# Performance work log

Measured on AMD Instinct MI355X. Metric: run time of the kernel, lower is better.

The kernel has to match this reference:

```python
import jax, jax.numpy as jnp
import numpy as np

T, H, I, E, S = 1024, 1024, 512, 64, 2  # tokens, hidden, intermediate, routed experts, shared experts
G, TOPK_GROUP, K = 8, 4, 8              # n_group, topk_group, num_experts_per_tok


def setup_inputs() -> dict:
    key = jax.random.key(0)
    ks = jax.random.split(key, 6)
    scale = 0.02
    x = jax.random.normal(ks[0], (T, H), dtype=jnp.float32)
    gate_w = jax.random.normal(ks[1], (E, H), dtype=jnp.float32) * scale   # MoEGate.weight [E,H]
    w_gu = jax.random.normal(ks[2], (E, H, 2 * I), dtype=jnp.float32) * scale  # gate_up_proj.weight.T per expert
    w_d = jax.random.normal(ks[3], (E, I, H), dtype=jnp.float32) * scale       # down_proj.weight.T per expert
    s_gu = jax.random.normal(ks[4], (S, H, 2 * I), dtype=jnp.float32) * scale  # shared experts
    s_d = jax.random.normal(ks[5], (S, I, H), dtype=jnp.float32) * scale
    return {"x": x, "gate_w": gate_w, "w_gu": w_gu, "w_d": w_d, "s_gu": s_gu, "s_d": s_d}


def _moe_forward(x, gate_w, w_gu, w_d, s_gu, s_d):
    t, h = x.shape
    e = w_gu.shape[0]
    i = w_gu.shape[2] // 2
    group_size = e // G

    # ---- shared experts (always active), summed ----
    sh = jnp.einsum('th,shf->stf', x, s_gu)            # [S,T,2I]
    shared = jnp.einsum('stf,sfh->th', jax.nn.silu(sh[..., :i]) * sh[..., i:], s_d)

    # ---- grouped top-k gating ----
    logits = x @ gate_w.T                               # [T,E]
    group_logits = logits.reshape(t, G, group_size)
    gw, gi = jax.lax.top_k(group_logits, TOPK_GROUP)    # [T,G,topk_group]
    gw = gw.reshape(t, G * TOPK_GROUP)
    gi = gi.reshape(t, G * TOPK_GROUP)
    topk_w, ti = jax.lax.top_k(gw, K)                   # [T,K]
    sel_group = ti // TOPK_GROUP
    expert_in_group = jnp.take_along_axis(gi, ti, axis=1)
    topk_idx = sel_group * group_size + expert_in_group # [T,K]
    topk_w = topk_w / (topk_w.sum(axis=-1, keepdims=True) + 1e-20)  # norm_topk_prob

    # ---- combine weights: sparse [T,E] scatter of top-k weights ----
    combine = jnp.zeros((t, e), x.dtype).at[jnp.arange(t)[:, None], topk_idx].add(topk_w)

    # ---- routed experts: dense grouped GEMM, zero-weighted where unselected ----
    gu = jnp.einsum('th,ehf->etf', x, w_gu)             # [E,T,2I]
    hidden = jax.nn.silu(gu[..., :i]) * gu[..., i:]     # [E,T,I]
    y = jnp.einsum('eti,eih->eth', hidden, w_d)         # [E,T,H]
    routed = jnp.einsum('eth,te->th', y, combine)

    return shared + routed


def reference(x, gate_w, w_gu, w_d, s_gu, s_d):
    return _moe_forward(x, gate_w, w_gu, w_d, s_gu, s_d)
```

## Files before the change

kernel.cpp:

```cpp
#include <hip/hip_runtime.h>
#include <hip/hip_bf16.h>

#define T_ 1024
#define H_ 1024
#define I_ 512
#define E_ 64
#define S_ 2
#define NJOB 66
#define KSEL 8
#define GRP 8
#define GSIZE 8
#define TKG 4
#define ROWS_TOTAL (T_*KSEL + S_*T_)

#define BM 128
#define BN 64
#define BK 32
#define LDA 40
#define LDB 40

typedef __attribute__((ext_vector_type(8))) __bf16 bf16x8;
typedef __attribute__((ext_vector_type(4))) float f32x4;

__device__ inline unsigned short f2bf(float f) {
    unsigned u = __float_as_uint(f);
    u += 0x7FFFu + ((u >> 16) & 1u);
    return (unsigned short)(u >> 16);
}

__global__ __launch_bounds__(256) void cvt_x_kernel(const float* __restrict__ x,
                                                    unsigned short* __restrict__ xb) {
    int i = (blockIdx.x * 256 + threadIdx.x) * 4;
    float4 v = *(const float4*)(x + i);
    ushort4 o;
    o.x = f2bf(v.x); o.y = f2bf(v.y); o.z = f2bf(v.z); o.w = f2bf(v.w);
    *(ushort4*)(xb + i) = o;
}

__global__ __launch_bounds__(64) void gate_kernel(const float* __restrict__ x,
                                                  const float* __restrict__ gate_w,
                                                  int* __restrict__ counts,
                                                  int* __restrict__ topk_idx,
                                                  float* __restrict__ topk_w) {
    int t = blockIdx.x;
    int e = threadIdx.x;
    const float4* xr = (const float4*)(x + (size_t)t * H_);
    const float4* wr = (const float4*)(gate_w + (size_t)e * H_);
    float acc = 0.0f;
    for (int i = 0; i < H_ / 4; ++i) {
        float4 a = xr[i], b = wr[i];
        acc += a.x * b.x + a.y * b.y + a.z * b.z + a.w * b.w;
    }
    __shared__ float lg[E_];
    lg[e] = acc;
    __syncthreads();
    if (e == 0) {
        float cv[GRP * TKG];
        int   ce[GRP * TKG];
        for (int g = 0; g < GRP; ++g) {
            unsigned used = 0;
            for (int r = 0; r < TKG; ++r) {
                float best = -INFINITY; int bi = 0;
                for (int j = 0; j < GSIZE; ++j) {
                    if (used & (1u << j)) continue;
                    float v = lg[g * GSIZE + j];
                    if (v > best) { best = v; bi = j; }
                }
                used |= 1u << bi;
                cv[g * TKG + r] = best;
                ce[g * TKG + r] = g * GSIZE + bi;
            }
        }
        float sv[KSEL]; int si[KSEL];
        unsigned used = 0;
        float sum = 0.0f;
        for (int r = 0; r < KSEL; ++r) {
            float best = -INFINITY; int bi = 0;
            for (int j = 0; j < GRP * TKG; ++j) {
                if (used & (1u << j)) continue;
                if (cv[j] > best) { best = cv[j]; bi = j; }
            }
            used |= 1u << bi;
            sv[r] = best; si[r] = ce[bi];
            sum += best;
        }
        float inv = 1.0f / (sum + 1e-20f);
        for (int r = 0; r < KSEL; ++r) {
            topk_idx[t * KSEL + r] = si[r];
            topk_w[t * KSEL + r] = sv[r] * inv;
            atomicAdd(&counts[si[r]], 1);
        }
    }
}

__global__ void prefix_kernel(int* __restrict__ counts, int* __restrict__ offsets,
                              int* __restrict__ cursor) {
    if (threadIdx.x == 0) {
        counts[E_] = T_;
        counts[E_ + 1] = T_;
        int acc = 0;
        for (int j = 0; j < NJOB; ++j) {
            offsets[j] = acc;
            cursor[j] = acc;
            acc += counts[j];
        }
        offsets[NJOB] = acc;
    }
}

__global__ __launch_bounds__(256) void place_kernel(const int* __restrict__ topk_idx,
                                                    const float* __restrict__ topk_w,
                                                    const int* __restrict__ offsets,
                                                    int* __restrict__ cursor,
                                                    int* __restrict__ row_token,
                                                    float* __restrict__ row_w) {
    int p = blockIdx.x * 256 + threadIdx.x;
    if (p < T_ * KSEL) {
        int t = p >> 3;
        int e = topk_idx[p];
        int slot = atomicAdd(&cursor[e], 1);
        row_token[slot] = t;
        row_w[slot] = topk_w[p];
    } else if (p < T_ * KSEL + S_ * T_) {
        int q = p - T_ * KSEL;
        int s = q >> 10;
        int t = q & (T_ - 1);
        int slot = offsets[E_ + s] + t;
        row_token[slot] = t;
        row_w[slot] = 1.0f;
    }
}

__global__ __launch_bounds__(256) void gateup_kernel(const unsigned short* __restrict__ xb,
                                                     const float* __restrict__ w_gu,
                                                     const float* __restrict__ s_gu,
                                                     const int* __restrict__ offsets,
                                                     const int* __restrict__ row_token,
                                                     unsigned short* __restrict__ hidden) {
    int job = blockIdx.x, mt = blockIdx.y, nt = blockIdx.z;
    int seg = offsets[job];
    int cnt = offsets[job + 1] - seg;
    int m0 = mt * BM;
    if (m0 >= cnt) return;
    const float* Bp = (job < E_) ? (w_gu + (size_t)job * H_ * (2 * I_))
                                 : (s_gu + (size_t)(job - E_) * H_ * (2 * I_));
    int n0 = nt * BN;

    __shared__ unsigned short As[BM * LDA];
    __shared__ unsigned short Bg[BN * LDB];
    __shared__ unsigned short Bu[BN * LDB];

    int tid = threadIdx.x;
    int wv = tid >> 6;
    int lane = tid & 63;
    int lrow = lane & 15;
    int lq = lane >> 4;

    int arow0 = tid >> 2;
    int akc = (tid & 3) * 8;
    int arow1 = (tid + 256) >> 2;
    int gidx0 = seg + m0 + arow0; if (gidx0 > ROWS_TOTAL - 1) gidx0 = ROWS_TOTAL - 1;
    int gidx1 = seg + m0 + arow1; if (gidx1 > ROWS_TOTAL - 1) gidx1 = ROWS_TOTAL - 1;
    const unsigned short* ap0 = xb + (size_t)row_token[gidx0] * H_;
    const unsigned short* ap1 = xb + (size_t)row_token[gidx1] * H_;

    int bk0 = tid >> 4;
    int bnc = (tid & 15) * 4;
    int bk1 = bk0 + 16;

    f32x4 accg[2][4], accu[2][4];
    f32x4 zero = {0.f, 0.f, 0.f, 0.f};
#pragma unroll
    for (int a = 0; a < 2; ++a)
#pragma unroll
        for (int b = 0; b < 4; ++b) { accg[a][b] = zero; accu[a][b] = zero; }

    for (int k0 = 0; k0 < H_; k0 += BK) {
        *(uint4*)&As[arow0 * LDA + akc] = *(const uint4*)(ap0 + k0 + akc);
        *(uint4*)&As[arow1 * LDA + akc] = *(const uint4*)(ap1 + k0 + akc);

        float4 vg0 = *(const float4*)(Bp + (size_t)(k0 + bk0) * (2 * I_) + n0 + bnc);
        float4 vg1 = *(const float4*)(Bp + (size_t)(k0 + bk1) * (2 * I_) + n0 + bnc);
        float4 vu0 = *(const float4*)(Bp + (size_t)(k0 + bk0) * (2 * I_) + (I_ + n0) + bnc);
        float4 vu1 = *(const float4*)(Bp + (size_t)(k0 + bk1) * (2 * I_) + (I_ + n0) + bnc);
        Bg[(bnc + 0) * LDB + bk0] = f2bf(vg0.x);
        Bg[(bnc + 1) * LDB + bk0] = f2bf(vg0.y);
        Bg[(bnc + 2) * LDB + bk0] = f2bf(vg0.z);
        Bg[(bnc + 3) * LDB + bk0] = f2bf(vg0.w);
        Bg[(bnc + 0) * LDB + bk1] = f2bf(vg1.x);
        Bg[(bnc + 1) * LDB + bk1] = f2bf(vg1.y);
        Bg[(bnc + 2) * LDB + bk1] = f2bf(vg1.z);
        Bg[(bnc + 3) * LDB + bk1] = f2bf(vg1.w);
        Bu[(bnc + 0) * LDB + bk0] = f2bf(vu0.x);
        Bu[(bnc + 1) * LDB + bk0] = f2bf(vu0.y);
        Bu[(bnc + 2) * LDB + bk0] = f2bf(vu0.z);
        Bu[(bnc + 3) * LDB + bk0] = f2bf(vu0.w);
        Bu[(bnc + 0) * LDB + bk1] = f2bf(vu1.x);
        Bu[(bnc + 1) * LDB + bk1] = f2bf(vu1.y);
        Bu[(bnc + 2) * LDB + bk1] = f2bf(vu1.z);
        Bu[(bnc + 3) * LDB + bk1] = f2bf(vu1.w);
        __syncthreads();

#pragma unroll
        for (int rb = 0; rb < 2; ++rb) {
            bf16x8 af = *(const bf16x8*)&As[(wv * 32 + rb * 16 + lrow) * LDA + lq * 8];
#pragma unroll
            for (int cb = 0; cb < 4; ++cb) {
                bf16x8 bg = *(const bf16x8*)&Bg[(cb * 16 + lrow) * LDB + lq * 8];
                bf16x8 bu = *(const bf16x8*)&Bu[(cb * 16 + lrow) * LDB + lq * 8];
                accg[rb][cb] = __builtin_amdgcn_mfma_f32_16x16x32_bf16(af, bg, accg[rb][cb], 0, 0, 0);
                accu[rb][cb] = __builtin_amdgcn_mfma_f32_16x16x32_bf16(af, bu, accu[rb][cb], 0, 0, 0);
            }
        }
        __syncthreads();
    }

#pragma unroll
    for (int rb = 0; rb < 2; ++rb) {
#pragma unroll
        for (int cb = 0; cb < 4; ++cb) {
#pragma unroll
            for (int r = 0; r < 4; ++r) {
                int row = wv * 32 + rb * 16 + lq * 4 + r;
                if (m0 + row < cnt) {
                    float g = accg[rb][cb][r];
                    float u = accu[rb][cb][r];
                    float h = g / (1.0f + __expf(-g)) * u;
                    int col = n0 + cb * 16 + lrow;
                    hidden[(size_t)(seg + m0 + row) * I_ + col] = f2bf(h);
                }
            }
        }
    }
}

__global__ __launch_bounds__(256) void down_kernel(const unsigned short* __restrict__ hidden,
                                                   const float* __restrict__ w_d,
                                                   const float* __restrict__ s_d,
                                                   const int* __restrict__ offsets,
                                                   const int* __restrict__ row_token,
                                                   const float* __restrict__ row_w,
                                                   float* __restrict__ out) {
    int job = blockIdx.x, mt = blockIdx.y, nt = blockIdx.z;
    int seg = offsets[job];
    int cnt = offsets[job + 1] - seg;
    int m0 = mt * BM;
    if (m0 >= cnt) return;
    const float* Bp = (job < E_) ? (w_d + (size_t)job * I_ * H_)
                                 : (s_d + (size_t)(job - E_) * I_ * H_);
    int n0 = nt * BN;

    __shared__ unsigned short As[BM * LDA];
    __shared__ unsigned short Bs[BN * LDB];

    int tid = threadIdx.x;
    int wv = tid >> 6;
    int lane = tid & 63;
    int lrow = lane & 15;
    int lq = lane >> 4;

    int arow0 = tid >> 2;
    int akc = (tid & 3) * 8;
    int arow1 = (tid + 256) >> 2;
    int gidx0 = seg + m0 + arow0; if (gidx0 > ROWS_TOTAL - 1) gidx0 = ROWS_TOTAL - 1;
    int gidx1 = seg + m0 + arow1; if (gidx1 > ROWS_TOTAL - 1) gidx1 = ROWS_TOTAL - 1;
    const unsigned short* ap0 = hidden + (size_t)gidx0 * I_;
    const unsigned short* ap1 = hidden + (size_t)gidx1 * I_;

    int bk0 = tid >> 4;
    int bnc = (tid & 15) * 4;
    int bk1 = bk0 + 16;

    f32x4 acc[2][4];
    f32x4 zero = {0.f, 0.f, 0.f, 0.f};
#pragma unroll
    for (int a = 0; a < 2; ++a)
#pragma unroll
        for (int b = 0; b < 4; ++b) acc[a][b] = zero;

    for (int k0 = 0; k0 < I_; k0 += BK) {
        *(uint4*)&As[arow0 * LDA + akc] = *(const uint4*)(ap0 + k0 + akc);
        *(uint4*)&As[arow1 * LDA + akc] = *(const uint4*)(ap1 + k0 + akc);

        float4 v0 = *(const float4*)(Bp + (size_t)(k0 + bk0) * H_ + n0 + bnc);
        float4 v1 = *(const float4*)(Bp + (size_t)(k0 + bk1) * H_ + n0 + bnc);
        Bs[(bnc + 0) * LDB + bk0] = f2bf(v0.x);
        Bs[(bnc + 1) * LDB + bk0] = f2bf(v0.y);
        Bs[(bnc + 2) * LDB + bk0] = f2bf(v0.z);
        Bs[(bnc + 3) * LDB + bk0] = f2bf(v0.w);
        Bs[(bnc + 0) * LDB + bk1] = f2bf(v1.x);
        Bs[(bnc + 1) * LDB + bk1] = f2bf(v1.y);
        Bs[(bnc + 2) * LDB + bk1] = f2bf(v1.z);
        Bs[(bnc + 3) * LDB + bk1] = f2bf(v1.w);
        __syncthreads();

#pragma unroll
        for (int rb = 0; rb < 2; ++rb) {
            bf16x8 af = *(const bf16x8*)&As[(wv * 32 + rb * 16 + lrow) * LDA + lq * 8];
#pragma unroll
            for (int cb = 0; cb < 4; ++cb) {
                bf16x8 bf = *(const bf16x8*)&Bs[(cb * 16 + lrow) * LDB + lq * 8];
                acc[rb][cb] = __builtin_amdgcn_mfma_f32_16x16x32_bf16(af, bf, acc[rb][cb], 0, 0, 0);
            }
        }
        __syncthreads();
    }

#pragma unroll
    for (int rb = 0; rb < 2; ++rb) {
#pragma unroll
        for (int cb = 0; cb < 4; ++cb) {
#pragma unroll
            for (int r = 0; r < 4; ++r) {
                int row = wv * 32 + rb * 16 + lq * 4 + r;
                if (m0 + row < cnt) {
                    int gi = seg + m0 + row;
                    float v = acc[rb][cb][r] * row_w[gi];
                    atomicAdd(&out[(size_t)row_token[gi] * H_ + n0 + cb * 16 + lrow], v);
                }
            }
        }
    }
}

extern "C" void kernel_launch(void* const* d_in, const int* in_sizes, int n_in,
                              void* d_out, int out_size, void* d_ws, size_t ws_size,
                              hipStream_t stream) {
    const float* x      = (const float*)d_in[0];
    const float* gate_w = (const float*)d_in[1];
    const float* w_gu   = (const float*)d_in[2];
    const float* w_d    = (const float*)d_in[3];
    const float* s_gu   = (const float*)d_in[4];
    const float* s_d    = (const float*)d_in[5];
    float* out = (float*)d_out;

    char* ws = (char*)d_ws;
    size_t off = 0;
    auto carve = [&](size_t bytes) -> void* {
        void* p = ws + off;
        off += (bytes + 255) & ~(size_t)255;
        return p;
    };
    int* counts            = (int*)carve(NJOB * 4);
    int* offsets           = (int*)carve((NJOB + 1) * 4);
    int* cursor            = (int*)carve(NJOB * 4);
    int* topk_idx          = (int*)carve(T_ * KSEL * 4);
    float* topk_w          = (float*)carve(T_ * KSEL * 4);
    int* row_token         = (int*)carve(ROWS_TOTAL * 4);
    float* row_w           = (float*)carve(ROWS_TOTAL * 4);
    unsigned short* xb     = (unsigned short*)carve((size_t)T_ * H_ * 2);
    unsigned short* hidden = (unsigned short*)carve((size_t)ROWS_TOTAL * I_ * 2);

    hipMemsetAsync(out, 0, (size_t)T_ * H_ * 4, stream);
    hipMemsetAsync(counts, 0, NJOB * 4, stream);

    cvt_x_kernel<<<(T_ * H_ / 4) / 256, 256, 0, stream>>>(x, xb);
    gate_kernel<<<T_, 64, 0, stream>>>(x, gate_w, counts, topk_idx, topk_w);
    prefix_kernel<<<1, 64, 0, stream>>>(counts, offsets, cursor);
    place_kernel<<<(ROWS_TOTAL + 255) / 256, 256, 0, stream>>>(topk_idx, topk_w, offsets,
                                                               cursor, row_token, row_w);
    gateup_kernel<<<dim3(NJOB, T_ / BM, I_ / BN), 256, 0, stream>>>(xb, w_gu, s_gu, offsets,
                                                                    row_token, hidden);
    down_kernel<<<dim3(NJOB, T_ / BM, H_ / BN), 256, 0, stream>>>(hidden, w_d, s_d, offsets,
                                                                  row_token, row_w, out);
}
```

Before: 703.0 us.

## Restructure GEMM kernels with register-prefetched weights, direct A loads, tiled gate

The gate-up and down GEMMs now read activation rows straight from global memory into MFMA registers, with no LDS staging. Weight tiles use BK=64, are prefetched one step ahead into registers, and are stored to LDS as packed vectors with staggered writes. The down kernel loads the token index and weight once per row before the atomic adds. The gate kernel handles four tokens per block and stages a transposed weight tile in LDS. This aims to cut LDS traffic, scalar stores and global latency stalls, at the cost of more registers and uncoalesced direct A loads.

```diff
diff --git a/kernel.cpp b/kernel.cpp
--- a/kernel.cpp
+++ b/kernel.cpp
@@ -15,11 +15,11 @@
 
 #define BM 128
 #define BN 64
-#define BK 32
-#define LDA 40
-#define LDB 40
+#define LDB 72
 
 typedef __attribute__((ext_vector_type(8))) __bf16 bf16x8;
+typedef __attribute__((ext_vector_type(8))) unsigned short u16x8;
+typedef __attribute__((ext_vector_type(4))) unsigned short u16x4;
 typedef __attribute__((ext_vector_type(4))) float f32x4;
 
 __device__ inline unsigned short f2bf(float f) {
@@ -31,30 +31,57 @@
 __global__ __launch_bounds__(256) void cvt_x_kernel(const float* __restrict__ x,
                                                     unsigned short* __restrict__ xb) {
     int i = (blockIdx.x * 256 + threadIdx.x) * 4;
-    float4 v = *(const float4*)(x + i);
-    ushort4 o;
-    o.x = f2bf(v.x); o.y = f2bf(v.y); o.z = f2bf(v.z); o.w = f2bf(v.w);
-    *(ushort4*)(xb + i) = o;
-}
-
-__global__ __launch_bounds__(64) void gate_kernel(const float* __restrict__ x,
-                                                  const float* __restrict__ gate_w,
-                                                  int* __restrict__ counts,
-                                                  int* __restrict__ topk_idx,
-                                                  float* __restrict__ topk_w) {
-    int t = blockIdx.x;
-    int e = threadIdx.x;
-    const float4* xr = (const float4*)(x + (size_t)t * H_);
-    const float4* wr = (const float4*)(gate_w + (size_t)e * H_);
-    float acc = 0.0f;
-    for (int i = 0; i < H_ / 4; ++i) {
-        float4 a = xr[i], b = wr[i];
-        acc += a.x * b.x + a.y * b.y + a.z * b.z + a.w * b.w;
-    }
-    __shared__ float lg[E_];
-    lg[e] = acc;
+    f32x4 v = *(const f32x4*)(x + i);
+    u16x4 o;
+    o[0] = f2bf(v[0]); o[1] = f2bf(v[1]); o[2] = f2bf(v[2]); o[3] = f2bf(v[3]);
+    *(u16x4*)(xb + i) = o;
+}
+
+__global__ __launch_bounds__(256) void gate_kernel(const float* __restrict__ x,
+                                                   const float* __restrict__ gate_w,
+                                                   int* __restrict__ counts,
+                                                   int* __restrict__ topk_idx,
+                                                   float* __restrict__ topk_w) {
+    __shared__ float Wt[64 * 65];
+    __shared__ float Xs[4 * 65];
+    __shared__ float lg[4 * 65];
+
+    int tid = threadIdx.x;
+    int t0 = blockIdx.x * 4;
+    int e = tid & 63;
+    int wq = tid >> 6;
+    int er = tid >> 2;
+    int kq = (tid & 3) * 16;
+    int xk = tid & 63;
+
+    float acc = 0.f;
+    for (int kc = 0; kc < 16; ++kc) {
+        const float* wp = gate_w + er * H_ + kc * 64 + kq;
+        f32x4 w0 = *(const f32x4*)(wp);
+        f32x4 w1 = *(const f32x4*)(wp + 4);
+        f32x4 w2 = *(const f32x4*)(wp + 8);
+        f32x4 w3 = *(const f32x4*)(wp + 12);
+        float xv = x[(size_t)(t0 + wq) * H_ + kc * 64 + xk];
+        __syncthreads();
+#pragma unroll
+        for (int i = 0; i < 4; ++i) {
+            Wt[(kq + i) * 65 + er] = w0[i];
+            Wt[(kq + 4 + i) * 65 + er] = w1[i];
+            Wt[(kq + 8 + i) * 65 + er] = w2[i];
+            Wt[(kq + 12 + i) * 65 + er] = w3[i];
+        }
+        Xs[wq * 65 + xk] = xv;
+        __syncthreads();
+#pragma unroll 8
+        for (int k = 0; k < 64; ++k)
+            acc += Wt[k * 65 + e] * Xs[wq * 65 + k];
+    }
+    lg[wq * 65 + e] = acc;
     __syncthreads();
-    if (e == 0) {
+
+    if (tid < 4) {
+        int t = t0 + tid;
+        const float* L = &lg[tid * 65];
         float cv[GRP * TKG];
         int   ce[GRP * TKG];
         for (int g = 0; g < GRP; ++g) {
@@ -63,7 +90,7 @@
                 float best = -INFINITY; int bi = 0;
                 for (int j = 0; j < GSIZE; ++j) {
                     if (used & (1u << j)) continue;
-                    float v = lg[g * GSIZE + j];
+                    float v = L[g * GSIZE + j];
                     if (v > best) { best = v; bi = j; }
                 }
                 used |= 1u << bi;
@@ -145,93 +172,101 @@
     const float* Bp = (job < E_) ? (w_gu + (size_t)job * H_ * (2 * I_))
                                  : (s_gu + (size_t)(job - E_) * H_ * (2 * I_));
     int n0 = nt * BN;
-
-    __shared__ unsigned short As[BM * LDA];
-    __shared__ unsigned short Bg[BN * LDB];
-    __shared__ unsigned short Bu[BN * LDB];
+    const int N2 = 2 * I_;
+
+    __shared__ unsigned short Bs[2 * BN * LDB];
 
     int tid = threadIdx.x;
-    int wv = tid >> 6;
-    int lane = tid & 63;
-    int lrow = lane & 15;
-    int lq = lane >> 4;
-
-    int arow0 = tid >> 2;
-    int akc = (tid & 3) * 8;
-    int arow1 = (tid + 256) >> 2;
-    int gidx0 = seg + m0 + arow0; if (gidx0 > ROWS_TOTAL - 1) gidx0 = ROWS_TOTAL - 1;
-    int gidx1 = seg + m0 + arow1; if (gidx1 > ROWS_TOTAL - 1) gidx1 = ROWS_TOTAL - 1;
-    const unsigned short* ap0 = xb + (size_t)row_token[gidx0] * H_;
-    const unsigned short* ap1 = xb + (size_t)row_token[gidx1] * H_;
-
-    int bk0 = tid >> 4;
-    int bnc = (tid & 15) * 4;
-    int bk1 = bk0 + 16;
-
-    f32x4 accg[2][4], accu[2][4];
+    int wv = tid >> 6, lane = tid & 63, lrow = lane & 15, lq = lane >> 4;
+
+    const unsigned short* arow[2];
+#pragma unroll
+    for (int rb = 0; rb < 2; ++rb) {
+        int r = m0 + wv * 32 + rb * 16 + lrow;
+        int gi = seg + (r < cnt ? r : 0);
+        arow[rb] = xb + (size_t)row_token[gi] * H_ + lq * 8;
+    }
+
+    int half = tid >> 7;
+    int h = tid & 127;
+    int nb = (h & 15) * 4;
+    int kb = (h >> 4) * 8;
+    const float* bgp = Bp + (size_t)kb * N2 + (half ? (I_ + n0) : n0) + nb;
+    unsigned short* wrow = &Bs[(half * BN + nb) * LDB + kb];
+    int stagger = tid & 3;
+
+    f32x4 acc[2][2][4];
     f32x4 zero = {0.f, 0.f, 0.f, 0.f};
 #pragma unroll
     for (int a = 0; a < 2; ++a)
 #pragma unroll
-        for (int b = 0; b < 4; ++b) { accg[a][b] = zero; accu[a][b] = zero; }
-
-    for (int k0 = 0; k0 < H_; k0 += BK) {
-        *(uint4*)&As[arow0 * LDA + akc] = *(const uint4*)(ap0 + k0 + akc);
-        *(uint4*)&As[arow1 * LDA + akc] = *(const uint4*)(ap1 + k0 + akc);
-
-        float4 vg0 = *(const float4*)(Bp + (size_t)(k0 + bk0) * (2 * I_) + n0 + bnc);
-        float4 vg1 = *(const float4*)(Bp + (size_t)(k0 + bk1) * (2 * I_) + n0 + bnc);
-        float4 vu0 = *(const float4*)(Bp + (size_t)(k0 + bk0) * (2 * I_) + (I_ + n0) + bnc);
-        float4 vu1 = *(const float4*)(Bp + (size_t)(k0 + bk1) * (2 * I_) + (I_ + n0) + bnc);
-        Bg[(bnc + 0) * LDB + bk0] = f2bf(vg0.x);
-        Bg[(bnc + 1) * LDB + bk0] = f2bf(vg0.y);
-        Bg[(bnc + 2) * LDB + bk0] = f2bf(vg0.z);
-        Bg[(bnc + 3) * LDB + bk0] = f2bf(vg0.w);
-        Bg[(bnc + 0) * LDB + bk1] = f2bf(vg1.x);
-        Bg[(bnc + 1) * LDB + bk1] = f2bf(vg1.y);
-        Bg[(bnc + 2) * LDB + bk1] = f2bf(vg1.z);
-        Bg[(bnc + 3) * LDB + bk1] = f2bf(vg1.w);
-        Bu[(bnc + 0) * LDB + bk0] = f2bf(vu0.x);
-        Bu[(bnc + 1) * LDB + bk0] = f2bf(vu0.y);
-        Bu[(bnc + 2) * LDB + bk0] = f2bf(vu0.z);
-        Bu[(bnc + 3) * LDB + bk0] = f2bf(vu0.w);
-        Bu[(bnc + 0) * LDB + bk1] = f2bf(vu1.x);
-        Bu[(bnc + 1) * LDB + bk1] = f2bf(vu1.y);
-        Bu[(bnc + 2) * LDB + bk1] = f2bf(vu1.z);
-        Bu[(bnc + 3) * LDB + bk1] = f2bf(vu1.w);
-        __syncthreads();
-
-#pragma unroll
-        for (int rb = 0; rb < 2; ++rb) {
-            bf16x8 af = *(const bf16x8*)&As[(wv * 32 + rb * 16 + lrow) * LDA + lq * 8];
-#pragma unroll
-            for (int cb = 0; cb < 4; ++cb) {
-                bf16x8 bg = *(const bf16x8*)&Bg[(cb * 16 + lrow) * LDB + lq * 8];
-                bf16x8 bu = *(const bf16x8*)&Bu[(cb * 16 + lrow) * LDB + lq * 8];
-                accg[rb][cb] = __builtin_amdgcn_mfma_f32_16x16x32_bf16(af, bg, accg[rb][cb], 0, 0, 0);
-                accu[rb][cb] = __builtin_amdgcn_mfma_f32_16x16x32_bf16(af, bu, accu[rb][cb], 0, 0, 0);
+        for (int b = 0; b < 2; ++b)
+#pragma unroll
+            for (int c = 0; c < 4; ++c) acc[a][b][c] = zero;
+
+    f32x4 bv[8];
+#pragma unroll
+    for (int j = 0; j < 8; ++j) bv[j] = *(const f32x4*)(bgp + (size_t)j * N2);
+
+    for (int kt = 0; kt < H_ / 64; ++kt) {
+        u16x8 pk[4];
+#pragma unroll
+        for (int c = 0; c < 4; ++c)
+#pragma unroll
+            for (int j = 0; j < 8; ++j) pk[c][j] = f2bf(bv[j][c]);
+        __syncthreads();
+#pragma unroll
+        for (int c0 = 0; c0 < 4; ++c0) {
+            int c = (c0 + stagger) & 3;
+            *(u16x8*)(wrow + c * LDB) = pk[c];
+        }
+        __syncthreads();
+
+        bf16x8 av[2][2];
+#pragma unroll
+        for (int rb = 0; rb < 2; ++rb)
+#pragma unroll
+            for (int kk = 0; kk < 2; ++kk)
+                av[rb][kk] = *(const bf16x8*)(arow[rb] + kt * 64 + kk * 32);
+
+        if (kt + 1 < H_ / 64) {
+#pragma unroll
+            for (int j = 0; j < 8; ++j)
+                bv[j] = *(const f32x4*)(bgp + (size_t)((kt + 1) * 64 + j) * N2);
+        }
+
+#pragma unroll
+        for (int kk = 0; kk < 2; ++kk) {
+#pragma unroll
+            for (int mat = 0; mat < 2; ++mat) {
+                bf16x8 bfr[4];
+#pragma unroll
+                for (int cb = 0; cb < 4; ++cb)
+                    bfr[cb] = *(const bf16x8*)&Bs[(mat * BN + cb * 16 + lrow) * LDB + kk * 32 + lq * 8];
+#pragma unroll
+                for (int rb = 0; rb < 2; ++rb)
+#pragma unroll
+                    for (int cb = 0; cb < 4; ++cb)
+                        acc[rb][mat][cb] = __builtin_amdgcn_mfma_f32_16x16x32_bf16(
+                            av[rb][kk], bfr[cb], acc[rb][mat][cb], 0, 0, 0);
             }
         }
-        __syncthreads();
-    }
-
-#pragma unroll
-    for (int rb = 0; rb < 2; ++rb) {
-#pragma unroll
-        for (int cb = 0; cb < 4; ++cb) {
+    }
+
+#pragma unroll
+    for (int rb = 0; rb < 2; ++rb)
+#pragma unroll
+        for (int cb = 0; cb < 4; ++cb)
 #pragma unroll
             for (int r = 0; r < 4; ++r) {
                 int row = wv * 32 + rb * 16 + lq * 4 + r;
                 if (m0 + row < cnt) {
-                    float g = accg[rb][cb][r];
-                    float u = accu[rb][cb][r];
-                    float h = g / (1.0f + __expf(-g)) * u;
-                    int col = n0 + cb * 16 + lrow;
-                    hidden[(size_t)(seg + m0 + row) * I_ + col] = f2bf(h);
+                    float g = acc[rb][0][cb][r];
+                    float u = acc[rb][1][cb][r];
+                    float hh = g / (1.0f + __expf(-g)) * u;
+                    hidden[(size_t)(seg + m0 + row) * I_ + n0 + cb * 16 + lrow] = f2bf(hh);
                 }
             }
-        }
-    }
 }
 
 __global__ __launch_bounds__(256) void down_kernel(const unsigned short* __restrict__ hidden,
@@ -250,77 +285,96 @@
                                  : (s_d + (size_t)(job - E_) * I_ * H_);
     int n0 = nt * BN;
 
-    __shared__ unsigned short As[BM * LDA];
     __shared__ unsigned short Bs[BN * LDB];
 
     int tid = threadIdx.x;
-    int wv = tid >> 6;
-    int lane = tid & 63;
-    int lrow = lane & 15;
-    int lq = lane >> 4;
-
-    int arow0 = tid >> 2;
-    int akc = (tid & 3) * 8;
-    int arow1 = (tid + 256) >> 2;
-    int gidx0 = seg + m0 + arow0; if (gidx0 > ROWS_TOTAL - 1) gidx0 = ROWS_TOTAL - 1;
-    int gidx1 = seg + m0 + arow1; if (gidx1 > ROWS_TOTAL - 1) gidx1 = ROWS_TOTAL - 1;
-    const unsigned short* ap0 = hidden + (size_t)gidx0 * I_;
-    const unsigned short* ap1 = hidden + (size_t)gidx1 * I_;
-
-    int bk0 = tid >> 4;
-    int bnc = (tid & 15) * 4;
-    int bk1 = bk0 + 16;
+    int wv = tid >> 6, lane = tid & 63, lrow = lane & 15, lq = lane >> 4;
+
+    const unsigned short* arow[2];
+    int arix[2];
+#pragma unroll
+    for (int rb = 0; rb < 2; ++rb) {
+        int r = m0 + wv * 32 + rb * 16 + lrow;
+        int gi = seg + (r < cnt ? r : 0);
+        arow[rb] = hidden + (size_t)gi * I_ + lq * 8;
+        arix[rb] = gi;
+        (void)arix;
+    }
+
+    int nb = (tid & 15) * 4;
+    int kb = (tid >> 4) * 4;
+    const float* bdp = Bp + (size_t)kb * H_ + n0 + nb;
+    unsigned short* wrow = &Bs[nb * LDB + kb];
+    int stagger = tid & 3;
 
     f32x4 acc[2][4];
     f32x4 zero = {0.f, 0.f, 0.f, 0.f};
 #pragma unroll
     for (int a = 0; a < 2; ++a)
 #pragma unroll
-        for (int b = 0; b < 4; ++b) acc[a][b] = zero;
-
-    for (int k0 = 0; k0 < I_; k0 += BK) {
-        *(uint4*)&As[arow0 * LDA + akc] = *(const uint4*)(ap0 + k0 + akc);
-        *(uint4*)&As[arow1 * LDA + akc] = *(const uint4*)(ap1 + k0 + akc);
-
-        float4 v0 = *(const float4*)(Bp + (size_t)(k0 + bk0) * H_ + n0 + bnc);
-        float4 v1 = *(const float4*)(Bp + (size_t)(k0 + bk1) * H_ + n0 + bnc);
-        Bs[(bnc + 0) * LDB + bk0] = f2bf(v0.x);
-        Bs[(bnc + 1) * LDB + bk0] = f2bf(v0.y);
-        Bs[(bnc + 2) * LDB + bk0] = f2bf(v0.z);
-        Bs[(bnc + 3) * LDB + bk0] = f2bf(v0.w);
-        Bs[(bnc + 0) * LDB + bk1] = f2bf(v1.x);
-        Bs[(bnc + 1) * LDB + bk1] = f2bf(v1.y);
-        Bs[(bnc + 2) * LDB + bk1] = f2bf(v1.z);
-        Bs[(bnc + 3) * LDB + bk1] = f2bf(v1.w);
-        __syncthreads();
-
-#pragma unroll
-        for (int rb = 0; rb < 2; ++rb) {
-            bf16x8 af = *(const bf16x8*)&As[(wv * 32 + rb * 16 + lrow) * LDA + lq * 8];
-#pragma unroll
-            for (int cb = 0; cb < 4; ++cb) {
-                bf16x8 bf = *(const bf16x8*)&Bs[(cb * 16 + lrow) * LDB + lq * 8];
-                acc[rb][cb] = __builtin_amdgcn_mfma_f32_16x16x32_bf16(af, bf, acc[rb][cb], 0, 0, 0);
+        for (int c = 0; c < 4; ++c) acc[a][c] = zero;
+
+    f32x4 bv[4];
+#pragma unroll
+    for (int j = 0; j < 4; ++j) bv[j] = *(const f32x4*)(bdp + (size_t)j * H_);
+
+    for (int kt = 0; kt < I_ / 64; ++kt) {
+        u16x4 pk[4];
+#pragma unroll
+        for (int c = 0; c < 4; ++c)
+#pragma unroll
+            for (int j = 0; j < 4; ++j) pk[c][j] = f2bf(bv[j][c]);
+        __syncthreads();
+#pragma unroll
+        for (int c0 = 0; c0 < 4; ++c0) {
+            int c = (c0 + stagger) & 3;
+            *(u16x4*)(wrow + c * LDB) = pk[c];
+        }
+        __syncthreads();
+
+        bf16x8 av[2][2];
+#pragma unroll
+        for (int rb = 0; rb < 2; ++rb)
+#pragma unroll
+            for (int kk = 0; kk < 2; ++kk)
+                av[rb][kk] = *(const bf16x8*)(arow[rb] + kt * 64 + kk * 32);
+
+        if (kt + 1 < I_ / 64) {
+#pragma unroll
+            for (int j = 0; j < 4; ++j)
+                bv[j] = *(const f32x4*)(bdp + (size_t)((kt + 1) * 64 + j) * H_);
+        }
+
+#pragma unroll
+        for (int kk = 0; kk < 2; ++kk) {
+            bf16x8 bfr[4];
+#pragma unroll
+            for (int cb = 0; cb < 4; ++cb)
+                bfr[cb] = *(const bf16x8*)&Bs[(cb * 16 + lrow) * LDB + kk * 32 + lq * 8];
+#pragma unroll
+            for (int rb = 0; rb < 2; ++rb)
+#pragma unroll
+                for (int cb = 0; cb < 4; ++cb)
+                    acc[rb][cb] = __builtin_amdgcn_mfma_f32_16x16x32_bf16(
+                        av[rb][kk], bfr[cb], acc[rb][cb], 0, 0, 0);
+        }
+    }
+
+#pragma unroll
+    for (int rb = 0; rb < 2; ++rb)
+#pragma unroll
+        for (int r = 0; r < 4; ++r) {
+            int row = wv * 32 + rb * 16 + lq * 4 + r;
+            if (m0 + row < cnt) {
+                int gi = seg + m0 + row;
+                int tok = row_token[gi];
+                float w = row_w[gi];
+#pragma unroll
+                for (int cb = 0; cb < 4; ++cb)
+                    atomicAdd(&out[(size_t)tok * H_ + n0 + cb * 16 + lrow],
+                              acc[rb][cb][r] * w);
             }
         }
-        __syncthreads();
-    }
-
-#pragma unroll
-    for (int rb = 0; rb < 2; ++rb) {
-#pragma unroll
-        for (int cb = 0; cb < 4; ++cb) {
-#pragma unroll
-            for (int r = 0; r < 4; ++r) {
-                int row = wv * 32 + rb * 16 + lq * 4 + r;
-                if (m0 + row < cnt) {
-                    int gi = seg + m0 + row;
-                    float v = acc[rb][cb][r] * row_w[gi];
-                    atomicAdd(&out[(size_t)row_token[gi] * H_ + n0 + cb * 16 + lrow], v);
-                }
-            }
-        }
-    }
 }
 
 extern "C" void kernel_launch(void* const* d_in, const int* in_sizes, int n_in,
@@ -355,7 +409,7 @@
     hipMemsetAsync(counts, 0, NJOB * 4, stream);
 
     cvt_x_kernel<<<(T_ * H_ / 4) / 256, 256, 0, stream>>>(x, xb);
-    gate_kernel<<<T_, 64, 0, stream>>>(x, gate_w, counts, topk_idx, topk_w);
+    gate_kernel<<<T_ / 4, 256, 0, stream>>>(x, gate_w, counts, topk_idx, topk_w);
     prefix_kernel<<<1, 64, 0, stream>>>(counts, offsets, cursor);
     place_kernel<<<(ROWS_TOTAL + 255) / 256, 256, 0, stream>>>(topk_idx, topk_w, offsets,
                                                                cursor, row_token, row_w);
```

Measured after the change: 853.4 us. 21.4% more time.
